# Performance work log

Measured on AMD Instinct MI355X. Metric: run time of the kernel, lower is better.

## Reference

```python
import jax, jax.numpy as jnp
import numpy as np

NUM_PATCHES = 4
PATCH_RADIUS = 0.2


def setup_inputs() -> dict:
    key = jax.random.key(0)
    points = jax.random.normal(key, (64, 65536, 6), dtype=jnp.float32)
    return {"points": points}


def _fps(xyz, n_samples):
    """Furthest point sampling (pointnet2 convention: start at index 0).
    xyz: (B, N, 3) -> (B, n_samples) int32 indices."""
    B, N, _ = xyz.shape

    def body(carry, _):
        min_d, last_idx = carry                                   # (B,N), (B,)
        last = jnp.take_along_axis(xyz, last_idx[:, None, None], axis=1)  # (B,1,3)
        d = jnp.sum((xyz - last) ** 2, axis=-1)                   # (B,N)
        min_d = jnp.minimum(min_d, d)
        nxt = jnp.argmax(min_d, axis=1).astype(jnp.int32)
        return (min_d, nxt), last_idx

    init = (jnp.full((B, N), 1e10, dtype=xyz.dtype),
            jnp.zeros((B,), dtype=jnp.int32))
    (_, _), idxs = jax.lax.scan(body, init, None, length=n_samples)
    return idxs.T                                                  # (B, n_samples)


def reference(points):
    B, N, C = points.shape
    xyz = points[..., :3]

    # 1) pick patch centers via FPS
    centers_idx = _fps(xyz, NUM_PATCHES)                           # (B,P)
    centers = jnp.take_along_axis(xyz, centers_idx[..., None], axis=1)  # (B,P,3)

    # 2) distance of every point to nearest center -> drop mask
    dist = jnp.linalg.norm(xyz[:, :, None, :] - centers[:, None, :, :], axis=-1)  # (B,N,P)
    min_dist = jnp.min(dist, axis=2)                               # (B,N)
    keep = min_dist >= PATCH_RADIUS                                # (B,N) bool, True = kept

    # 3) stable compaction: kept points first (original order preserved),
    #    then repeat-fill pattern valid_points[j % num_valid]
    order = jnp.argsort(jnp.logical_not(keep).astype(jnp.int32), axis=1, stable=True)  # (B,N)
    num_valid = jnp.sum(keep, axis=1)                              # (B,)
    j = jnp.arange(N, dtype=jnp.int32)[None, :]                    # (1,N)
    k = j % jnp.maximum(num_valid, 1)[:, None]                     # (B,N)
    src = jnp.take_along_axis(order, k, axis=1)                    # (B,N)
    out = jnp.take_along_axis(points, src[..., None], axis=1)      # (B,N,C)

    # all points dropped -> zeros (matches torch branch)
    return jnp.where((num_valid > 0)[:, None, None], out, jnp.zeros_like(out))
```

## Files before the change

kernel.cpp:

```cpp
#include <hip/hip_runtime.h>
#include <stdint.h>

#define NN 65536
#define BB 64
#define TPB 256

#define BPB 16
#define GRID_BLKS (BB * BPB)
#define PPB 4096
#define LPT 16
#define WPB (PPB / 64)

#define FBPB 32
#define FGRID (BB * FBPB)
#define FPPB 2048
#define FLPT 8
#define GBPB 16
#define GGRID (BB * GBPB)
#define GLPT 16

__device__ __forceinline__ void cstore64(unsigned long long* p, unsigned long long v) {
    __hip_atomic_store(p, v, __ATOMIC_RELAXED, __HIP_MEMORY_SCOPE_AGENT);
}
__device__ __forceinline__ unsigned long long cload64(const unsigned long long* p) {
    return __hip_atomic_load(p, __ATOMIC_RELAXED, __HIP_MEMORY_SCOPE_AGENT);
}

__device__ __forceinline__ float sqdist(float x, float y, float z,
                                        float cx, float cy, float cz) {
    float dx = __fsub_rn(x, cx);
    float dy = __fsub_rn(y, cy);
    float dz = __fsub_rn(z, cz);
    return __fadd_rn(__fadd_rn(__fmul_rn(dx, dx), __fmul_rn(dy, dy)),
                     __fmul_rn(dz, dz));
}

__device__ __forceinline__ unsigned long long pack_key(float v, int i) {
    return ((unsigned long long)__float_as_uint(v) << 32) |
           (unsigned long long)(0xFFFFFFFFu - (unsigned)i);
}
__device__ __forceinline__ int key_idx(unsigned long long key) {
    return (int)(0xFFFFFFFFu - (unsigned)(key & 0xFFFFFFFFu));
}

__device__ __forceinline__ int sel_bit(uint64_t m, int r) {
    int bit = 0;
    int c = __popcll(m & 0xFFFFFFFFull);
    if (r >= c) { r -= c; m >>= 32; bit += 32; }
    c = __popcll(m & 0xFFFFull);
    if (r >= c) { r -= c; m >>= 16; bit += 16; }
    c = __popcll(m & 0xFFull);
    if (r >= c) { r -= c; m >>= 8; bit += 8; }
    c = __popcll(m & 0xFull);
    if (r >= c) { r -= c; m >>= 4; bit += 4; }
    c = __popcll(m & 0x3ull);
    if (r >= c) { r -= c; m >>= 2; bit += 2; }
    if (r >= (int)(m & 1ull)) { bit += 1; }
    return bit;
}

template<int NB>
__device__ __forceinline__ void batch_barrier(unsigned* cnt, unsigned* gen) {
    __syncthreads();
    if (threadIdx.x == 0) {
        unsigned g = __hip_atomic_load(gen, __ATOMIC_RELAXED,
                                       __HIP_MEMORY_SCOPE_AGENT);
        unsigned a = __hip_atomic_fetch_add(cnt, 1u, __ATOMIC_ACQ_REL,
                                            __HIP_MEMORY_SCOPE_AGENT) + 1u;
        if (a == (unsigned)NB) {
            __hip_atomic_store(cnt, 0u, __ATOMIC_RELAXED,
                               __HIP_MEMORY_SCOPE_AGENT);
            __hip_atomic_store(gen, g + 1u, __ATOMIC_RELEASE,
                               __HIP_MEMORY_SCOPE_AGENT);
        } else {
            while (__hip_atomic_load(gen, __ATOMIC_RELAXED,
                                     __HIP_MEMORY_SCOPE_AGENT) == g)
                __builtin_amdgcn_s_sleep(4);
        }
    }
    __syncthreads();
}

__global__ void init_barrier(unsigned* bar) {
    const int t = threadIdx.x;
    bar[t * 32 + 0] = 0u;
    bar[t * 32 + 1] = 0u;
}

union Shm {
    float2 xy[PPB];
    struct { uint64_t m[1024]; int pre[1024]; } e;
};

__global__ __launch_bounds__(TPB, 4) void fused_kernel(
        const float* __restrict__ pts,
        unsigned long long* __restrict__ partKey,
        uint64_t* __restrict__ masks,
        float* __restrict__ out,
        unsigned* __restrict__ bar) {
    const int gb = blockIdx.x;
    const int b = gb >> 4, blk = gb & 15;
    const int tid = threadIdx.x;
    const int lane = tid & 63, wid = tid >> 6;
    const float* base = pts + (size_t)b * NN * 6;
    unsigned* bcnt = bar + b * 32;
    unsigned* bgen = bar + b * 32 + 1;

    __shared__ Shm shm;
    __shared__ unsigned long long s_k[4];
    __shared__ int s_ws[4], s_wo[4];
    __shared__ int s_nv;

    const float c0x = base[0], c0y = base[1], c0z = base[2];
    float z[LPT], md[LPT];
    #pragma unroll
    for (int l = 0; l < LPT; ++l) {
        const int q = l * TPB + tid;
        const int p = blk * PPB + q;
        const float* src = base + (size_t)p * 6;
        float2 xy = *(const float2*)src;
        shm.xy[q] = xy;
        z[l] = src[2];
        md[l] = sqdist(xy.x, xy.y, z[l], c0x, c0y, c0z);
    }
    #pragma unroll
    for (int l = 0; l < LPT; ++l) asm volatile("" : "+v"(z[l]));

    for (int k = 0; k < 3; ++k) {
        float bestv = -1.0f; int besti = 0x7fffffff;
        #pragma unroll
        for (int l = 0; l < LPT; ++l) {
            if (md[l] > bestv) { bestv = md[l]; besti = blk * PPB + l * TPB + tid; }
        }
        unsigned long long key = pack_key(bestv, besti);
        #pragma unroll
        for (int off = 32; off > 0; off >>= 1) {
            unsigned long long ok = __shfl_down(key, off, 64);
            if (ok > key) key = ok;
        }
        if (lane == 0) s_k[wid] = key;
        __syncthreads();
        if (tid == 0) {
            unsigned long long bk = s_k[0];
            #pragma unroll
            for (int w = 1; w < 4; ++w) bk = (s_k[w] > bk) ? s_k[w] : bk;
            cstore64(&partKey[k * GRID_BLKS + gb], bk);
        }
        batch_barrier<BPB>(bcnt, bgen);

        const unsigned long long* s = partKey + k * GRID_BLKS + b * BPB;
        unsigned long long bk = cload64(&s[lane & (BPB - 1)]);
        #pragma unroll
        for (int off = 32; off > 0; off >>= 1) {
            unsigned long long ok = __shfl_xor(bk, off, 64);
            if (ok > bk) bk = ok;
        }
        const float* cp = base + (size_t)key_idx(bk) * 6;
        const float cx = cp[0], cy = cp[1], cz = cp[2];
        #pragma unroll
        for (int l = 0; l < LPT; ++l) {
            float2 xy = shm.xy[l * TPB + tid];
            md[l] = fminf(md[l], sqdist(xy.x, xy.y, z[l], cx, cy, cz));
        }
    }

    uint64_t* mb = masks + (size_t)b * 1024;
    #pragma unroll
    for (int l = 0; l < LPT; ++l) {
        int keep = (__fsqrt_rn(md[l]) >= 0.2f) ? 1 : 0;
        uint64_t m = __ballot(keep);
        if (lane == 0)
            cstore64((unsigned long long*)&mb[blk * WPB + l * 4 + wid], m);
    }
    batch_barrier<BPB>(bcnt, bgen);

    uint64_t w[4];
    int cnt = 0;
    #pragma unroll
    for (int kk = 0; kk < 4; ++kk) {
        w[kk] = cload64((const unsigned long long*)&mb[tid * 4 + kk]);
        shm.e.m[tid * 4 + kk] = w[kk];
        cnt += __popcll(w[kk]);
    }
    int incl = cnt;
    #pragma unroll
    for (int off = 1; off < 64; off <<= 1) {
        int v = __shfl_up(incl, off, 64);
        if (lane >= off) incl += v;
    }
    if (lane == 63) s_ws[wid] = incl;
    __syncthreads();
    if (tid == 0) {
        int run = 0;
        #pragma unroll
        for (int q = 0; q < 4; ++q) { s_wo[q] = run; run += s_ws[q]; }
        s_nv = run;
    }
    __syncthreads();
    int run = s_wo[wid] + incl - cnt;
    #pragma unroll
    for (int kk = 0; kk < 4; ++kk) {
        shm.e.pre[tid * 4 + kk] = run;
        run += __popcll(w[kk]);
    }
    __syncthreads();

    const int nv = s_nv;
    float* ob = out + (size_t)b * NN * 6;

    if (nv <= 0) {
        float2 zz = make_float2(0.f, 0.f);
        #pragma unroll
        for (int l = 0; l < LPT; ++l) {
            int j = blk * PPB + l * TPB + tid;
            float2* o = (float2*)(ob + (size_t)j * 6);
            o[0] = zz; o[1] = zz; o[2] = zz;
        }
        return;
    }

    #pragma unroll
    for (int l = 0; l < LPT; ++l) {
        const int p = blk * PPB + l * TPB + tid;
        const int w_idx = blk * WPB + l * 4 + wid;
        uint64_t m = shm.e.m[w_idx];
        int rank = shm.e.pre[w_idx] + __popcll(m & ((1ull << lane) - 1ull));
        if ((m >> lane) & 1ull) {
            const float2* q = (const float2*)(base + (size_t)p * 6);
            float2* o = (float2*)(ob + (size_t)rank * 6);
            float2 r0 = q[0], r1 = q[1], r2 = q[2];
            o[0] = r0; o[1] = r1; o[2] = r2;
        }
    }

    const int T = NN - nv;
    if (T > 0) {
        const int chunk = (T + BPB - 1) / BPB;
        const int j0 = nv + blk * chunk;
        const int j1 = (j0 + chunk < NN) ? (j0 + chunk) : NN;
        for (int j = j0 + tid; j < j1; j += TPB) {
            unsigned jj = (unsigned)j % (unsigned)nv;
            int wd = 0;
            #pragma unroll
            for (int s2 = 512; s2 > 0; s2 >>= 1) {
                int cand = wd + s2;
                if (cand < 1024 && shm.e.pre[cand] <= (int)jj) wd = cand;
            }
            int src = wd * 64 + sel_bit(shm.e.m[wd], (int)jj - shm.e.pre[wd]);
            const float2* q = (const float2*)(base + (size_t)src * 6);
            float2* o = (float2*)(ob + (size_t)j * 6);
            float2 r0 = q[0], r1 = q[1], r2 = q[2];
            o[0] = r0; o[1] = r1; o[2] = r2;
        }
    }
}

__device__ __forceinline__ int reduce_part(const unsigned long long* partKey,
                                           int a, int b) {
    const unsigned long long* s = partKey + a * FGRID + b * FBPB;
    unsigned long long bk = s[0];
    #pragma unroll
    for (int w = 1; w < FBPB; ++w) bk = (s[w] > bk) ? s[w] : bk;
    return key_idx(bk);
}

template<int NC>
__global__ __launch_bounds__(TPB) void fps_pass(
        const float* __restrict__ pts, unsigned long long* partKey) {
    const int gb = blockIdx.x;
    const int b = gb >> 5, blk = gb & 31;
    const int tid = threadIdx.x;
    const int lane = tid & 63, wid = tid >> 6;
    const float* base = pts + (size_t)b * NN * 6;

    float cx[NC], cy[NC], cz[NC];
    cx[0] = base[0]; cy[0] = base[1]; cz[0] = base[2];
    #pragma unroll
    for (int k = 1; k < NC; ++k) {
        int idx = reduce_part(partKey, k - 1, b);
        const float* p = base + (size_t)idx * 6;
        cx[k] = p[0]; cy[k] = p[1]; cz[k] = p[2];
    }

    float bestv = -1.0f; int besti = 0x7fffffff;
    #pragma unroll
    for (int l = 0; l < FLPT; ++l) {
        const int p = blk * FPPB + l * TPB + tid;
        const float* q = base + (size_t)p * 6;
        float2 xy = *(const float2*)q;
        float  zz = q[2];
        float d = sqdist(xy.x, xy.y, zz, cx[0], cy[0], cz[0]);
        #pragma unroll
        for (int k = 1; k < NC; ++k)
            d = fminf(d, sqdist(xy.x, xy.y, zz, cx[k], cy[k], cz[k]));
        if (d > bestv) { bestv = d; besti = p; }
    }
    unsigned long long key = pack_key(bestv, besti);
    #pragma unroll
    for (int off = 32; off > 0; off >>= 1) {
        unsigned long long ok = __shfl_down(key, off, 64);
        if (ok > key) key = ok;
    }
    __shared__ unsigned long long s_k[4];
    if (lane == 0) s_k[wid] = key;
    __syncthreads();
    if (tid == 0) {
        unsigned long long bk = s_k[0];
        #pragma unroll
        for (int w = 1; w < 4; ++w) bk = (s_k[w] > bk) ? s_k[w] : bk;
        partKey[(NC - 1) * FGRID + gb] = bk;
    }
}

__global__ __launch_bounds__(TPB) void fps_final(
        const float* __restrict__ pts,
        const unsigned long long* __restrict__ partKey,
        uint64_t* __restrict__ masks) {
    const int gb = blockIdx.x;
    const int b = gb >> 5, blk = gb & 31;
    const int tid = threadIdx.x;
    const int lane = tid & 63, wid = tid >> 6;
    const float* base = pts + (size_t)b * NN * 6;

    float cx[4], cy[4], cz[4];
    cx[0] = base[0]; cy[0] = base[1]; cz[0] = base[2];
    #pragma unroll
    for (int k = 1; k < 4; ++k) {
        int idx = reduce_part(partKey, k - 1, b);
        const float* p = base + (size_t)idx * 6;
        cx[k] = p[0]; cy[k] = p[1]; cz[k] = p[2];
    }
    uint64_t* mb = masks + (size_t)b * 1024;

    #pragma unroll
    for (int l = 0; l < FLPT; ++l) {
        const int p = blk * FPPB + l * TPB + tid;
        const float* q = base + (size_t)p * 6;
        float2 xy = *(const float2*)q;
        float  zz = q[2];
        float d = sqdist(xy.x, xy.y, zz, cx[0], cy[0], cz[0]);
        #pragma unroll
        for (int k = 1; k < 4; ++k)
            d = fminf(d, sqdist(xy.x, xy.y, zz, cx[k], cy[k], cz[k]));
        int keep = (__fsqrt_rn(d) >= 0.2f) ? 1 : 0;
        uint64_t m = __ballot(keep);
        if (lane == 0) mb[blk * 32 + l * 4 + wid] = m;
    }
}

__global__ __launch_bounds__(TPB) void gather_kernel(
        const float* __restrict__ pts, const uint64_t* __restrict__ masks,
        float* __restrict__ out) {
    const int gb = blockIdx.x;
    const int b = gb >> 4, blk = gb & 15;
    const int tid = threadIdx.x;
    const int lane = tid & 63, wid = tid >> 6;
    __shared__ uint64_t s_m[1024];
    __shared__ int s_pre[1024];
    __shared__ int s_ws[4], s_wo[4];
    __shared__ int s_nv;

    const uint64_t* mb = masks + (size_t)b * 1024;
    uint64_t w[4];
    int cnt = 0;
    #pragma unroll
    for (int k = 0; k < 4; ++k) {
        w[k] = mb[tid * 4 + k];
        s_m[tid * 4 + k] = w[k];
        cnt += __popcll(w[k]);
    }
    int incl = cnt;
    #pragma unroll
    for (int off = 1; off < 64; off <<= 1) {
        int v = __shfl_up(incl, off, 64);
        if (lane >= off) incl += v;
    }
    if (lane == 63) s_ws[wid] = incl;
    __syncthreads();
    if (tid == 0) {
        int run = 0;
        #pragma unroll
        for (int q = 0; q < 4; ++q) { s_wo[q] = run; run += s_ws[q]; }
        s_nv = run;
    }
    __syncthreads();
    int run = s_wo[wid] + incl - cnt;
    #pragma unroll
    for (int k = 0; k < 4; ++k) {
        s_pre[tid * 4 + k] = run;
        run += __popcll(w[k]);
    }
    __syncthreads();

    const int nv = s_nv;
    const float* baseP = pts + (size_t)b * NN * 6;
    float* ob = out + (size_t)b * NN * 6;

    if (nv <= 0) {
        float2 zz = make_float2(0.f, 0.f);
        #pragma unroll
        for (int l = 0; l < GLPT; ++l) {
            int j = blk * 4096 + l * TPB + tid;
            float2* o = (float2*)(ob + (size_t)j * 6);
            o[0] = zz; o[1] = zz; o[2] = zz;
        }
        return;
    }

    #pragma unroll
    for (int l = 0; l < GLPT; ++l) {
        int j = blk * 4096 + l * TPB + tid;
        int jj = (int)((unsigned)j % (unsigned)nv);
        int wd = 0;
        #pragma unroll
        for (int s = 512; s > 0; s >>= 1) {
            int cand = wd + s;
            if (cand < 1024 && s_pre[cand] <= jj) wd = cand;
        }
        int src = wd * 64 + sel_bit(s_m[wd], jj - s_pre[wd]);
        const float2* p = (const float2*)(baseP + (size_t)src * 6);
        float2* o = (float2*)(ob + (size_t)j * 6);
        float2 r0 = p[0], r1 = p[1], r2 = p[2];
        o[0] = r0; o[1] = r1; o[2] = r2;
    }
}

extern "C" void kernel_launch(void* const* d_in, const int* in_sizes, int n_in,
                              void* d_out, int out_size, void* d_ws, size_t ws_size,
                              hipStream_t stream) {
    const float* pts = (const float*)d_in[0];
    float* out = (float*)d_out;

    unsigned long long* partKey = (unsigned long long*)d_ws;
    unsigned* bar = (unsigned*)((char*)d_ws + (48 << 10));
    uint64_t* masks = (uint64_t*)((char*)d_ws + (64 << 10));

    static int mode = -1;
    if (mode < 0) {
        int dev = 0;
        (void)hipGetDevice(&dev);
        int ncu = 0, nb = 0;
        hipError_t e1 = hipDeviceGetAttribute(&ncu, hipDeviceAttributeMultiprocessorCount, dev);
        hipError_t e2 = hipOccupancyMaxActiveBlocksPerMultiprocessor(
            &nb, (const void*)fused_kernel, TPB, 0);
        mode = (e1 == hipSuccess && e2 == hipSuccess &&
                (long)nb * (long)ncu >= (long)GRID_BLKS) ? 1 : 0;
    }

    if (mode == 1) {
        init_barrier<<<1, 64, 0, stream>>>(bar);
        fused_kernel<<<GRID_BLKS, TPB, 0, stream>>>(pts, partKey, masks, out, bar);
    } else {
        fps_pass<1><<<FGRID, TPB, 0, stream>>>(pts, partKey);
        fps_pass<2><<<FGRID, TPB, 0, stream>>>(pts, partKey);
        fps_pass<3><<<FGRID, TPB, 0, stream>>>(pts, partKey);
        fps_final<<<FGRID, TPB, 0, stream>>>(pts, partKey, masks);
        gather_kernel<<<GGRID, TPB, 0, stream>>>(pts, masks, out);
    }
}
```

Before: 246.0 us.

## Stage point loads through LDS for coalesced reads in fused kernel

Each wavefront now owns a contiguous 1024-point range and loads it in fully coalesced float2 chunks into an LDS staging buffer, then transposes to per-lane points. This replaces strided 24-byte-per-lane global reads. The point-to-mask-word mapping is changed to match the new per-wave layout, and the compaction pass reloads through the same staging path. The zero-fill path is also made contiguous. It adds LDS traffic and possible bank conflicts on the stride-3 reads, and drops the reuse of cached rows in favour of a second coalesced global read.

```diff
diff --git a/kernel.cpp b/kernel.cpp
--- a/kernel.cpp
+++ b/kernel.cpp
@@ -10,6 +10,7 @@
 #define PPB 4096
 #define LPT 16
 #define WPB (PPB / 64)
+#define WPW 16
 
 #define FBPB 32
 #define FGRID (BB * FBPB)
@@ -107,30 +108,43 @@
     unsigned* bgen = bar + b * 32 + 1;
 
     __shared__ Shm shm;
+    __shared__ float2 stage[4][192];
     __shared__ unsigned long long s_k[4];
     __shared__ int s_ws[4], s_wo[4];
     __shared__ int s_nv;
 
+    const int wbase = blk * PPB + wid * 1024;
+    const float2* wsrc = (const float2*)(base + (size_t)wbase * 6);
+
     const float c0x = base[0], c0y = base[1], c0z = base[2];
     float z[LPT], md[LPT];
     #pragma unroll
-    for (int l = 0; l < LPT; ++l) {
-        const int q = l * TPB + tid;
-        const int p = blk * PPB + q;
-        const float* src = base + (size_t)p * 6;
-        float2 xy = *(const float2*)src;
-        shm.xy[q] = xy;
-        z[l] = src[2];
-        md[l] = sqdist(xy.x, xy.y, z[l], c0x, c0y, c0z);
-    }
-    #pragma unroll
-    for (int l = 0; l < LPT; ++l) asm volatile("" : "+v"(z[l]));
+    for (int c = 0; c < LPT; ++c) {
+        const float2* src = wsrc + c * 192;
+        float2 v0 = src[lane];
+        float2 v1 = src[lane + 64];
+        float2 v2 = src[lane + 128];
+        stage[wid][lane      ] = v0;
+        stage[wid][lane + 64 ] = v1;
+        stage[wid][lane + 128] = v2;
+        float2 a  = stage[wid][lane * 3];
+        float2 b2 = stage[wid][lane * 3 + 1];
+        const int q = wid * 1024 + c * 64 + lane;
+        shm.xy[q] = a;
+        z[c] = b2.x;
+        md[c] = sqdist(a.x, a.y, b2.x, c0x, c0y, c0z);
+    }
+    #pragma unroll
+    for (int c = 0; c < LPT; ++c) asm volatile("" : "+v"(z[c]));
 
     for (int k = 0; k < 3; ++k) {
         float bestv = -1.0f; int besti = 0x7fffffff;
         #pragma unroll
-        for (int l = 0; l < LPT; ++l) {
-            if (md[l] > bestv) { bestv = md[l]; besti = blk * PPB + l * TPB + tid; }
+        for (int c = 0; c < LPT; ++c) {
+            if (md[c] > bestv) {
+                bestv = md[c];
+                besti = blk * PPB + wid * 1024 + c * 64 + lane;
+            }
         }
         unsigned long long key = pack_key(bestv, besti);
         #pragma unroll
@@ -158,19 +172,19 @@
         const float* cp = base + (size_t)key_idx(bk) * 6;
         const float cx = cp[0], cy = cp[1], cz = cp[2];
         #pragma unroll
-        for (int l = 0; l < LPT; ++l) {
-            float2 xy = shm.xy[l * TPB + tid];
-            md[l] = fminf(md[l], sqdist(xy.x, xy.y, z[l], cx, cy, cz));
+        for (int c = 0; c < LPT; ++c) {
+            float2 a = shm.xy[wid * 1024 + c * 64 + lane];
+            md[c] = fminf(md[c], sqdist(a.x, a.y, z[c], cx, cy, cz));
         }
     }
 
     uint64_t* mb = masks + (size_t)b * 1024;
     #pragma unroll
-    for (int l = 0; l < LPT; ++l) {
-        int keep = (__fsqrt_rn(md[l]) >= 0.2f) ? 1 : 0;
+    for (int c = 0; c < LPT; ++c) {
+        int keep = (__fsqrt_rn(md[c]) >= 0.2f) ? 1 : 0;
         uint64_t m = __ballot(keep);
         if (lane == 0)
-            cstore64((unsigned long long*)&mb[blk * WPB + l * 4 + wid], m);
+            cstore64((unsigned long long*)&mb[blk * WPB + wid * WPW + c], m);
     }
     batch_barrier<BPB>(bcnt, bgen);
 
@@ -210,25 +224,28 @@
 
     if (nv <= 0) {
         float2 zz = make_float2(0.f, 0.f);
-        #pragma unroll
-        for (int l = 0; l < LPT; ++l) {
-            int j = blk * PPB + l * TPB + tid;
-            float2* o = (float2*)(ob + (size_t)j * 6);
-            o[0] = zz; o[1] = zz; o[2] = zz;
-        }
+        float2* od = (float2*)(ob + (size_t)blk * PPB * 6);
+        for (int i = tid; i < PPB * 3; i += TPB) od[i] = zz;
         return;
     }
 
     #pragma unroll
-    for (int l = 0; l < LPT; ++l) {
-        const int p = blk * PPB + l * TPB + tid;
-        const int w_idx = blk * WPB + l * 4 + wid;
+    for (int c = 0; c < LPT; ++c) {
+        const float2* src = wsrc + c * 192;
+        float2 v0 = src[lane];
+        float2 v1 = src[lane + 64];
+        float2 v2 = src[lane + 128];
+        stage[wid][lane      ] = v0;
+        stage[wid][lane + 64 ] = v1;
+        stage[wid][lane + 128] = v2;
+        float2 r0 = stage[wid][lane * 3];
+        float2 r1 = stage[wid][lane * 3 + 1];
+        float2 r2 = stage[wid][lane * 3 + 2];
+        const int w_idx = blk * WPB + wid * WPW + c;
         uint64_t m = shm.e.m[w_idx];
         int rank = shm.e.pre[w_idx] + __popcll(m & ((1ull << lane) - 1ull));
         if ((m >> lane) & 1ull) {
-            const float2* q = (const float2*)(base + (size_t)p * 6);
             float2* o = (float2*)(ob + (size_t)rank * 6);
-            float2 r0 = q[0], r1 = q[1], r2 = q[2];
             o[0] = r0; o[1] = r1; o[2] = r2;
         }
     }
```

After: 247.1 us. About the same (+0.4%).
